# Kernel optimization log

Measured on AMD Instinct MI355X. Metric: run time of the kernel, lower is better.

Reference implementation:

```python
import jax, jax.numpy as jnp
import numpy as np
from jax import lax

B, T, D, H, HODE = 1024, 128, 64, 256, 256
DT = 0.1  # times spaced by 0.1 == integration_step_size -> one RK4 step per interval


def setup_inputs() -> dict:
    key = jax.random.key(0)
    ks = jax.random.split(key, 10)
    s = lambda fan: 1.0 / np.sqrt(fan)
    return {
        "x": jax.random.normal(ks[0], (B, T, D), jnp.float32),
        "times": jnp.arange(T, dtype=jnp.float32) * DT,
        "mask": (jax.random.uniform(ks[1], (B, T)) > 0.3).astype(jnp.float32),
        # ODE MLP: Linear(H->HODE), ReLU, Linear(HODE->H)
        "W1": jax.random.uniform(ks[2], (HODE, H), jnp.float32, -s(H), s(H)),
        "b1": jax.random.uniform(ks[3], (HODE,), jnp.float32, -s(H), s(H)),
        "W2": jax.random.uniform(ks[4], (H, HODE), jnp.float32, -s(HODE), s(HODE)),
        "b2": jax.random.uniform(ks[5], (H,), jnp.float32, -s(HODE), s(HODE)),
        # GRUCell params (torch layout: [3H, D]/[3H, H], gate order r,z,n)
        "W_ih": jax.random.uniform(ks[6], (3 * H, D), jnp.float32, -s(H), s(H)),
        "b_ih": jax.random.uniform(ks[7], (3 * H,), jnp.float32, -s(H), s(H)),
        "W_hh": jax.random.uniform(ks[8], (3 * H, H), jnp.float32, -s(H), s(H)),
        "b_hh": jax.random.uniform(ks[9], (3 * H,), jnp.float32, -s(H), s(H)),
    }


def _ode_gru_forward(x, times, mask, W1, b1, W2, b2, W_ih, b_ih, W_hh, b_hh):
    Bs, Ts, _ = x.shape
    Hs = W_hh.shape[1]

    def f(h):  # autonomous ODE vector field: MLP(h)
        return jnp.maximum(h @ W1.T + b1, 0.0) @ W2.T + b2

    def rk4_step(h, dt):
        k1 = f(h)
        k2 = f(h + 0.5 * dt * k1)
        k3 = f(h + 0.5 * dt * k2)
        k4 = f(h + dt * k3)
        return h + (dt / 6.0) * (k1 + 2.0 * k2 + 2.0 * k3 + k4)

    def gru_update(xt, h, m):
        gi = xt @ W_ih.T + b_ih  # [B, 3H]
        gh = h @ W_hh.T + b_hh
        i_r, i_z, i_n = jnp.split(gi, 3, axis=-1)
        h_r, h_z, h_n = jnp.split(gh, 3, axis=-1)
        r = jax.nn.sigmoid(i_r + h_r)
        z = jax.nn.sigmoid(i_z + h_z)
        n = jnp.tanh(i_n + r * h_n)
        h_next = (1.0 - z) * n + z * h
        m = m[:, None]
        return m * h_next + (1.0 - m) * h

    h0 = gru_update(x[:, 0], jnp.zeros((Bs, Hs), x.dtype), mask[:, 0])
    dts = times[1:] - times[:-1]  # [T-1]

    def step(h, inp):
        xt, mt, dt = inp
        h_ode = rk4_step(h, dt)
        h = gru_update(xt, h_ode, mt)
        return h, h

    xs = (jnp.swapaxes(x[:, 1:], 0, 1), jnp.swapaxes(mask[:, 1:], 0, 1), dts)
    _, hs = lax.scan(step, h0, xs)  # hs: [T-1, B, H]
    out = jnp.concatenate([h0[None], hs], axis=0)  # [T, B, H]
    return jnp.swapaxes(out, 0, 1)  # [B, T, H]


def reference(x, times, mask, W1, b1, W2, b2, W_ih, b_ih, W_hh, b_hh):
    return _ode_gru_forward(x, times, mask, W1, b1, W2, b2, W_ih, b_ih, W_hh, b_hh)
```

## Files before the change

kernel.cpp:

```cpp
#include <hip/hip_runtime.h>
#include <math.h>

#define TT_ 128
#define DD 64
#define HH 256
#define BB 16
#define NBLK 64
#define NTHR 1024

#define SA 260
#define SB 264
#define SXB 72

typedef short bf16x8 __attribute__((ext_vector_type(8)));
typedef float f32x4 __attribute__((ext_vector_type(4)));
typedef unsigned int uint;
typedef unsigned short ushort;

__device__ ushort g_W1p[16 * 8 * 2 * 512];
__device__ ushort g_W2p[16 * 8 * 2 * 512];
__device__ ushort g_Wrzp[32 * 10 * 2 * 512];
__device__ ushort g_Whnp[16 * 8 * 2 * 512];
__device__ ushort g_Winp[16 * 2 * 512];

__device__ __forceinline__ ushort bf16_rne(float f) {
  uint u = __builtin_bit_cast(uint, f);
  return (ushort)((u + 0x7fffu + ((u >> 16) & 1u)) >> 16);
}
__device__ __forceinline__ float bf16_f32(ushort h) {
  uint u = ((uint)h) << 16;
  return __builtin_bit_cast(float, u);
}
__device__ __forceinline__ void hl_split(float f, ushort& hi, ushort& lo) {
  const uint u = __builtin_bit_cast(uint, f);
  hi = (ushort)(u >> 16);
  const float fh = __builtin_bit_cast(float, u & 0xffff0000u);
  lo = (ushort)(__builtin_bit_cast(uint, f - fh) >> 16);
}

__global__ __launch_bounds__(256) void prep(
    const float* __restrict__ W1, const float* __restrict__ W2,
    const float* __restrict__ Wih, const float* __restrict__ Whh)
{
  const int s = blockIdx.x * 256 + threadIdx.x;
  const int S1 = 16 * 8 * 512;
  const int S2 = S1 + 16 * 8 * 512;
  const int S3 = S2 + 32 * 10 * 512;
  const int S4 = S3 + 16 * 8 * 512;
  const int S5 = S4 + 16 * 2 * 512;
  if (s >= S5) return;

  if (s < S2) {
    const int r = (s < S1) ? s : s - S1;
    const int t = r / (8 * 512);
    const int o = (r / 512) & 7;
    const int pos = r & 511;
    const int l = pos >> 3, j = pos & 7;
    const int n = t * 16 + (l & 15);
    const int k = o * 32 + (l >> 4) * 8 + j;
    const float w = (s < S1) ? W1[n * HH + k] : W2[n * HH + k];
    ushort hi = bf16_rne(w);
    ushort lo = bf16_rne(w - bf16_f32(hi));
    ushort* dst = (s < S1) ? g_W1p : g_W2p;
    dst[((t * 8 + o) * 2) * 512 + pos] = hi;
    dst[((t * 8 + o) * 2 + 1) * 512 + pos] = lo;
  } else if (s < S3) {
    const int r = s - S2;
    const int t = r / (10 * 512);
    const int o = (r / 512) % 10;
    const int pos = r & 511;
    const int l = pos >> 3, j = pos & 7;
    const int n = t * 16 + (l & 15);
    float w;
    if (o < 8) w = Whh[n * HH + o * 32 + (l >> 4) * 8 + j];
    else       w = Wih[n * DD + (o - 8) * 32 + (l >> 4) * 8 + j];
    ushort hi = bf16_rne(w);
    ushort lo = bf16_rne(w - bf16_f32(hi));
    g_Wrzp[((t * 10 + o) * 2) * 512 + pos] = hi;
    g_Wrzp[((t * 10 + o) * 2 + 1) * 512 + pos] = lo;
  } else if (s < S4) {
    const int r = s - S3;
    const int t = r / (8 * 512);
    const int o = (r / 512) & 7;
    const int pos = r & 511;
    const int l = pos >> 3, j = pos & 7;
    const int n = 512 + t * 16 + (l & 15);
    const float w = Whh[n * HH + o * 32 + (l >> 4) * 8 + j];
    ushort hi = bf16_rne(w);
    ushort lo = bf16_rne(w - bf16_f32(hi));
    g_Whnp[((t * 8 + o) * 2) * 512 + pos] = hi;
    g_Whnp[((t * 8 + o) * 2 + 1) * 512 + pos] = lo;
  } else {
    const int r = s - S4;
    const int t = r / (2 * 512);
    const int o = (r / 512) & 1;
    const int pos = r & 511;
    const int l = pos >> 3, j = pos & 7;
    const int n = 512 + t * 16 + (l & 15);
    const float w = Wih[n * DD + o * 32 + (l >> 4) * 8 + j];
    g_Winp[(t * 2 + o) * 512 + pos] = bf16_rne(w);
  }
}

#define MFMA(A, B, C) __builtin_amdgcn_mfma_f32_16x16x32_bf16((A), (B), (C), 0, 0, 0)

#define LBAR() asm volatile("s_waitcnt lgkmcnt(0)\ns_barrier" ::: "memory")

__device__ __forceinline__ f32x4 mm1(const ushort* __restrict__ Ahi,
                                     const ushort* __restrict__ Alo,
                                     const ushort* __restrict__ pack,
                                     int tile, int lane, f32x4 acc)
{
  const int aoff = (lane & 15) * SB + (lane >> 4) * 8;
  const ushort* wp = pack + (size_t)tile * 8192 + lane * 8;
#pragma unroll
  for (int o = 0; o < 8; ++o) {
    const bf16x8 ah = *(const bf16x8*)(Ahi + aoff + o * 32);
    const bf16x8 al = *(const bf16x8*)(Alo + aoff + o * 32);
    const bf16x8 wh = *(const bf16x8*)(wp + o * 1024);
    const bf16x8 wl = *(const bf16x8*)(wp + o * 1024 + 512);
    acc = MFMA(ah, wh, acc);
    acc = MFMA(al, wh, acc);
    acc = MFMA(ah, wl, acc);
  }
  return acc;
}

__device__ __forceinline__ void mm_rz(const ushort* __restrict__ Ahi,
                                      const ushort* __restrict__ Alo,
                                      const ushort* __restrict__ Xhi,
                                      const ushort* __restrict__ Xlo,
                                      int wv, int lane, f32x4& ar, f32x4& az)
{
  const int aoff = (lane & 15) * SB + (lane >> 4) * 8;
  const int xoff = (lane & 15) * SXB + (lane >> 4) * 8;
  const ushort* pr = g_Wrzp + (size_t)wv * 10240 + lane * 8;
  const ushort* pz = g_Wrzp + (size_t)(16 + wv) * 10240 + lane * 8;
#pragma unroll
  for (int o = 0; o < 8; ++o) {
    const bf16x8 ah = *(const bf16x8*)(Ahi + aoff + o * 32);
    const bf16x8 al = *(const bf16x8*)(Alo + aoff + o * 32);
    const bf16x8 wrh = *(const bf16x8*)(pr + o * 1024);
    const bf16x8 wrl = *(const bf16x8*)(pr + o * 1024 + 512);
    const bf16x8 wzh = *(const bf16x8*)(pz + o * 1024);
    const bf16x8 wzl = *(const bf16x8*)(pz + o * 1024 + 512);
    ar = MFMA(ah, wrh, ar); az = MFMA(ah, wzh, az);
    ar = MFMA(al, wrh, ar); az = MFMA(al, wzh, az);
    ar = MFMA(ah, wrl, ar); az = MFMA(ah, wzl, az);
  }
#pragma unroll
  for (int o = 0; o < 2; ++o) {
    const bf16x8 xh = *(const bf16x8*)(Xhi + xoff + o * 32);
    const bf16x8 xl = *(const bf16x8*)(Xlo + xoff + o * 32);
    const bf16x8 wrh = *(const bf16x8*)(pr + (8 + o) * 1024);
    const bf16x8 wzh = *(const bf16x8*)(pz + (8 + o) * 1024);
    ar = MFMA(xh, wrh, ar); az = MFMA(xh, wzh, az);
    ar = MFMA(xl, wrh, ar); az = MFMA(xl, wzh, az);
  }
}

__device__ __forceinline__ f32x4 mm_in(const ushort* __restrict__ Xhi,
                                       const ushort* __restrict__ Xlo,
                                       int wv, int lane, f32x4 acc)
{
  const int xoff = (lane & 15) * SXB + (lane >> 4) * 8;
  const ushort* pw = g_Winp + (size_t)wv * 1024 + lane * 8;
#pragma unroll
  for (int o = 0; o < 2; ++o) {
    const bf16x8 xh = *(const bf16x8*)(Xhi + xoff + o * 32);
    const bf16x8 xl = *(const bf16x8*)(Xlo + xoff + o * 32);
    const bf16x8 w = *(const bf16x8*)(pw + o * 512);
    acc = MFMA(xh, w, acc);
    acc = MFMA(xl, w, acc);
  }
  return acc;
}

__global__ __launch_bounds__(NTHR) void odegru_kernel(
    const float* __restrict__ x, const float* __restrict__ times,
    const float* __restrict__ mask,
    const float* __restrict__ b1, const float* __restrict__ b2,
    const float* __restrict__ bih, const float* __restrict__ bhh,
    float* __restrict__ out)
{
  __shared__ __align__(16) float sAh[BB * SA];
  __shared__ __align__(16) float sAin[BB * SA];
  __shared__ __align__(16) ushort sAhh[BB * SB], sAhl[BB * SB];
  __shared__ __align__(16) ushort sAinh[BB * SB], sAinl[BB * SB];
  __shared__ __align__(16) ushort sUh[BB * SB], sUl[BB * SB];
  __shared__ __align__(16) ushort sXh[BB * SXB], sXl[BB * SXB];
  __shared__ __align__(16) float sM[BB * TT_];

  const int tid = threadIdx.x;
  const int lane = tid & 63;
  const int wv = tid >> 6;
  const int l15 = lane & 15;
  const int lq = lane >> 4;
  const int b0 = blockIdx.x * BB;

  const int c = wv * 16 + l15;
  const float b1c = b1[c];
  const float b2c = b2[c];
  const float brz_r = bih[c] + bhh[c];
  const float brz_z = bih[c + 256] + bhh[c + 256];
  const float bn_i = bih[c + 512];
  const float bn_h = bhh[c + 512];

  const f32x4 Z = {0.f, 0.f, 0.f, 0.f};

  sM[tid] = mask[(size_t)b0 * TT_ + tid];
  sM[tid + 1024] = mask[(size_t)b0 * TT_ + tid + 1024];

  auto feval = [&](const ushort* Ahi, const ushort* Alo, f32x4& kv) {
    f32x4 a = mm1(Ahi, Alo, g_W1p, wv, lane, Z);
#pragma unroll
    for (int q = 0; q < 4; ++q) {
      const int b = lq * 4 + q;
      const float u = fmaxf(a[q] + b1c, 0.f);
      ushort hi, lo; hl_split(u, hi, lo);
      sUh[b * SB + c] = hi;
      sUl[b * SB + c] = lo;
    }
    LBAR();
    f32x4 p = mm1(sUh, sUl, g_W2p, wv, lane, Z);
    kv = p + b2c;
  };

  auto wAin = [&](float coef, const f32x4& v) {
#pragma unroll
    for (int q = 0; q < 4; ++q) {
      const int b = lq * 4 + q;
      const float nv = sAh[b * SA + c] + coef * v[q];
      sAin[b * SA + c] = nv;
      ushort hi, lo; hl_split(nv, hi, lo);
      sAinh[b * SB + c] = hi;
      sAinl[b * SB + c] = lo;
    }
  };

  for (int t = 0; t < TT_; ++t) {
    {
      const int b = tid >> 6, d = tid & 63;
      const float v = x[((size_t)(b0 + b) * TT_ + t) * DD + d];
      ushort hi, lo; hl_split(v, hi, lo);
      sXh[b * SXB + d] = hi;
      sXl[b * SXB + d] = lo;
    }
    if (t == 0) {
      const int cc = tid & 255;
#pragma unroll
      for (int q = 0; q < 4; ++q) {
        const int b = (tid >> 8) * 4 + q;
        sAin[b * SA + cc] = 0.f;
        sAinh[b * SB + cc] = 0;
        sAinl[b * SB + cc] = 0;
      }
    }
    LBAR();

    if (t > 0) {
      const float dtv = times[t] - times[t - 1];
      f32x4 kv, ks;
      feval(sAhh, sAhl, kv);
      ks = kv;
      wAin(0.5f * dtv, kv);
      LBAR();
      feval(sAinh, sAinl, kv);
      ks += 2.0f * kv;
      wAin(0.5f * dtv, kv);
      LBAR();
      feval(sAinh, sAinl, kv);
      ks += 2.0f * kv;
      wAin(dtv, kv);
      LBAR();
      feval(sAinh, sAinl, kv);
      ks += kv;
      wAin(dtv * (1.0f / 6.0f), ks);
      LBAR();
    }

    {
      f32x4 ar = Z, az = Z;
      mm_rz(sAinh, sAinl, sXh, sXl, wv, lane, ar, az);
      f32x4 ahn = mm1(sAinh, sAinl, g_Whnp, wv, lane, Z);
      f32x4 ain = mm_in(sXh, sXl, wv, lane, Z);

#pragma unroll
      for (int q = 0; q < 4; ++q) {
        const int b = lq * 4 + q;
        const float gr = ar[q] + brz_r;
        const float gz = az[q] + brz_z;
        const float hn = ahn[q] + bn_h;
        const float gn = ain[q] + bn_i;
        const float hode = sAin[b * SA + c];
        const float rg = 1.f / (1.f + __expf(-gr));
        const float zg = 1.f / (1.f + __expf(-gz));
        const float ng = 1.f - 2.f / (__expf(2.f * (gn + rg * hn)) + 1.f);
        const float hnext = (1.f - zg) * ng + zg * hode;
        const float m = sM[b * TT_ + t];
        const float hnew = m * hnext + (1.f - m) * hode;
        out[((size_t)(b0 + b) * TT_ + t) * HH + c] = hnew;
        sAh[b * SA + c] = hnew;
        ushort hi, lo; hl_split(hnew, hi, lo);
        sAhh[b * SB + c] = hi;
        sAhl[b * SB + c] = lo;
      }
    }
    LBAR();
  }
}

extern "C" void kernel_launch(void* const* d_in, const int* in_sizes, int n_in,
                              void* d_out, int out_size, void* d_ws, size_t ws_size,
                              hipStream_t stream) {
  (void)in_sizes; (void)n_in; (void)d_ws; (void)ws_size; (void)out_size;
  const float* x     = (const float*)d_in[0];
  const float* times = (const float*)d_in[1];
  const float* mask  = (const float*)d_in[2];
  const float* W1    = (const float*)d_in[3];
  const float* b1    = (const float*)d_in[4];
  const float* W2    = (const float*)d_in[5];
  const float* b2    = (const float*)d_in[6];
  const float* Wih   = (const float*)d_in[7];
  const float* bih   = (const float*)d_in[8];
  const float* Whh   = (const float*)d_in[9];
  const float* bhh   = (const float*)d_in[10];
  float* out = (float*)d_out;

  hipLaunchKernelGGL(prep, dim3((376832 + 255) / 256), dim3(256), 0, stream,
                     W1, W2, Wih, Whh);
  hipLaunchKernelGGL(odegru_kernel, dim3(NBLK), dim3(NTHR), 0, stream,
                     x, times, mask, b1, b2, bih, bhh, out);
}
```

Baseline: 6.858 ms.

## Prefetch packed weights each step, split MFMA accumulators, fuse GRU gate matmuls

At the start of every timestep, each wave issues global_load_lds prefetches of all its packed weight tiles into a dummy LDS buffer, so the weights are pulled into cache before the dependent MFMA chains read them from global memory. The matmul helpers now use two independent accumulators to shorten MFMA dependency chains. The r/z/n hidden-gate matmuls are fused into one loop with six accumulators, and the mask is stored transposed in LDS. The prefetches add memory traffic and instructions per step, and the extra accumulators raise register pressure.

```diff
diff --git a/kernel.cpp b/kernel.cpp
--- a/kernel.cpp
+++ b/kernel.cpp
@@ -106,74 +106,40 @@
 
 #define LBAR() asm volatile("s_waitcnt lgkmcnt(0)\ns_barrier" ::: "memory")
 
+__device__ __forceinline__ void pfq(const ushort* g, ushort* lds) {
+  __builtin_amdgcn_global_load_lds(
+      (const __attribute__((address_space(1))) void*)g,
+      (__attribute__((address_space(3))) void*)lds,
+      16, 0, 0);
+}
+__device__ __forceinline__ void pf_t16(const ushort* base, ushort* d) {
+#pragma unroll
+  for (int o = 0; o < 8; ++o) {
+    pfq(base + o * 1024, d);
+    pfq(base + o * 1024 + 512, d);
+  }
+}
+
 __device__ __forceinline__ f32x4 mm1(const ushort* __restrict__ Ahi,
                                      const ushort* __restrict__ Alo,
                                      const ushort* __restrict__ pack,
-                                     int tile, int lane, f32x4 acc)
+                                     int tile, int lane, int aoff, f32x4 acc)
 {
-  const int aoff = (lane & 15) * SB + (lane >> 4) * 8;
   const ushort* wp = pack + (size_t)tile * 8192 + lane * 8;
+  f32x4 a0 = acc;
+  f32x4 a1 = {0.f, 0.f, 0.f, 0.f};
 #pragma unroll
   for (int o = 0; o < 8; ++o) {
+    const bf16x8 wh = *(const bf16x8*)(wp + o * 1024);
+    const bf16x8 wl = *(const bf16x8*)(wp + o * 1024 + 512);
     const bf16x8 ah = *(const bf16x8*)(Ahi + aoff + o * 32);
     const bf16x8 al = *(const bf16x8*)(Alo + aoff + o * 32);
-    const bf16x8 wh = *(const bf16x8*)(wp + o * 1024);
-    const bf16x8 wl = *(const bf16x8*)(wp + o * 1024 + 512);
-    acc = MFMA(ah, wh, acc);
-    acc = MFMA(al, wh, acc);
-    acc = MFMA(ah, wl, acc);
-  }
-  return acc;
-}
-
-__device__ __forceinline__ void mm_rz(const ushort* __restrict__ Ahi,
-                                      const ushort* __restrict__ Alo,
-                                      const ushort* __restrict__ Xhi,
-                                      const ushort* __restrict__ Xlo,
-                                      int wv, int lane, f32x4& ar, f32x4& az)
-{
-  const int aoff = (lane & 15) * SB + (lane >> 4) * 8;
-  const int xoff = (lane & 15) * SXB + (lane >> 4) * 8;
-  const ushort* pr = g_Wrzp + (size_t)wv * 10240 + lane * 8;
-  const ushort* pz = g_Wrzp + (size_t)(16 + wv) * 10240 + lane * 8;
-#pragma unroll
-  for (int o = 0; o < 8; ++o) {
-    const bf16x8 ah = *(const bf16x8*)(Ahi + aoff + o * 32);
-    const bf16x8 al = *(const bf16x8*)(Alo + aoff + o * 32);
-    const bf16x8 wrh = *(const bf16x8*)(pr + o * 1024);
-    const bf16x8 wrl = *(const bf16x8*)(pr + o * 1024 + 512);
-    const bf16x8 wzh = *(const bf16x8*)(pz + o * 1024);
-    const bf16x8 wzl = *(const bf16x8*)(pz + o * 1024 + 512);
-    ar = MFMA(ah, wrh, ar); az = MFMA(ah, wzh, az);
-    ar = MFMA(al, wrh, ar); az = MFMA(al, wzh, az);
-    ar = MFMA(ah, wrl, ar); az = MFMA(ah, wzl, az);
-  }
-#pragma unroll
-  for (int o = 0; o < 2; ++o) {
-    const bf16x8 xh = *(const bf16x8*)(Xhi + xoff + o * 32);
-    const bf16x8 xl = *(const bf16x8*)(Xlo + xoff + o * 32);
-    const bf16x8 wrh = *(const bf16x8*)(pr + (8 + o) * 1024);
-    const bf16x8 wzh = *(const bf16x8*)(pz + (8 + o) * 1024);
-    ar = MFMA(xh, wrh, ar); az = MFMA(xh, wzh, az);
-    ar = MFMA(xl, wrh, ar); az = MFMA(xl, wzh, az);
-  }
-}
-
-__device__ __forceinline__ f32x4 mm_in(const ushort* __restrict__ Xhi,
-                                       const ushort* __restrict__ Xlo,
-                                       int wv, int lane, f32x4 acc)
-{
-  const int xoff = (lane & 15) * SXB + (lane >> 4) * 8;
-  const ushort* pw = g_Winp + (size_t)wv * 1024 + lane * 8;
-#pragma unroll
-  for (int o = 0; o < 2; ++o) {
-    const bf16x8 xh = *(const bf16x8*)(Xhi + xoff + o * 32);
-    const bf16x8 xl = *(const bf16x8*)(Xlo + xoff + o * 32);
-    const bf16x8 w = *(const bf16x8*)(pw + o * 512);
-    acc = MFMA(xh, w, acc);
-    acc = MFMA(xl, w, acc);
-  }
-  return acc;
+    f32x4& ac = (o & 1) ? a1 : a0;
+    ac = MFMA(ah, wh, ac);
+    ac = MFMA(al, wh, ac);
+    ac = MFMA(ah, wl, ac);
+  }
+  return a0 + a1;
 }
 
 __global__ __launch_bounds__(NTHR) void odegru_kernel(
@@ -189,7 +155,8 @@
   __shared__ __align__(16) ushort sAinh[BB * SB], sAinl[BB * SB];
   __shared__ __align__(16) ushort sUh[BB * SB], sUl[BB * SB];
   __shared__ __align__(16) ushort sXh[BB * SXB], sXl[BB * SXB];
-  __shared__ __align__(16) float sM[BB * TT_];
+  __shared__ __align__(16) float sMt[TT_ * BB];
+  __shared__ __align__(16) ushort sDummy[512];
 
   const int tid = threadIdx.x;
   const int lane = tid & 63;
@@ -197,6 +164,8 @@
   const int l15 = lane & 15;
   const int lq = lane >> 4;
   const int b0 = blockIdx.x * BB;
+  const int aoff = l15 * SB + lq * 8;
+  const int xoff = l15 * SXB + lq * 8;
 
   const int c = wv * 16 + l15;
   const float b1c = b1[c];
@@ -208,11 +177,21 @@
 
   const f32x4 Z = {0.f, 0.f, 0.f, 0.f};
 
-  sM[tid] = mask[(size_t)b0 * TT_ + tid];
-  sM[tid + 1024] = mask[(size_t)b0 * TT_ + tid + 1024];
+  const ushort* W1b = g_W1p + (size_t)wv * 8192 + lane * 8;
+  const ushort* W2b = g_W2p + (size_t)wv * 8192 + lane * 8;
+  const ushort* Wrb = g_Wrzp + (size_t)wv * 10240 + lane * 8;
+  const ushort* Wzb = g_Wrzp + (size_t)(16 + wv) * 10240 + lane * 8;
+  const ushort* Whb = g_Whnp + (size_t)wv * 8192 + lane * 8;
+  const ushort* Wib = g_Winp + (size_t)wv * 1024 + lane * 8;
+
+  {
+    const int e0 = tid, e1 = tid + 1024;
+    sMt[(e0 & 127) * BB + (e0 >> 7)] = mask[(size_t)(b0 + (e0 >> 7)) * TT_ + (e0 & 127)];
+    sMt[(e1 & 127) * BB + (e1 >> 7)] = mask[(size_t)(b0 + (e1 >> 7)) * TT_ + (e1 & 127)];
+  }
 
   auto feval = [&](const ushort* Ahi, const ushort* Alo, f32x4& kv) {
-    f32x4 a = mm1(Ahi, Alo, g_W1p, wv, lane, Z);
+    f32x4 a = mm1(Ahi, Alo, g_W1p, wv, lane, aoff, Z);
 #pragma unroll
     for (int q = 0; q < 4; ++q) {
       const int b = lq * 4 + q;
@@ -222,7 +201,7 @@
       sUl[b * SB + c] = lo;
     }
     LBAR();
-    f32x4 p = mm1(sUh, sUl, g_W2p, wv, lane, Z);
+    f32x4 p = mm1(sUh, sUl, g_W2p, wv, lane, aoff, Z);
     kv = p + b2c;
   };
 
@@ -246,6 +225,13 @@
       sXh[b * SXB + d] = hi;
       sXl[b * SXB + d] = lo;
     }
+    pf_t16(W1b, sDummy);
+    pf_t16(W2b, sDummy);
+    pf_t16(Wrb, sDummy); pfq(Wrb + 8 * 1024, sDummy); pfq(Wrb + 9 * 1024, sDummy);
+    pf_t16(Wzb, sDummy); pfq(Wzb + 8 * 1024, sDummy); pfq(Wzb + 9 * 1024, sDummy);
+    pf_t16(Whb, sDummy);
+    pfq(Wib, sDummy); pfq(Wib + 512, sDummy);
+
     if (t == 0) {
       const int cc = tid & 255;
 #pragma unroll
@@ -280,10 +266,36 @@
     }
 
     {
-      f32x4 ar = Z, az = Z;
-      mm_rz(sAinh, sAinl, sXh, sXl, wv, lane, ar, az);
-      f32x4 ahn = mm1(sAinh, sAinl, g_Whnp, wv, lane, Z);
-      f32x4 ain = mm_in(sXh, sXl, wv, lane, Z);
+      f32x4 r0 = Z, r1 = Z, z0 = Z, z1 = Z, h0 = Z, h1 = Z;
+#pragma unroll
+      for (int o = 0; o < 8; ++o) {
+        const int ac = aoff + o * 32;
+        const bf16x8 ah = *(const bf16x8*)(sAinh + ac);
+        const bf16x8 al = *(const bf16x8*)(sAinl + ac);
+        const bf16x8 wrh = *(const bf16x8*)(Wrb + o * 1024);
+        const bf16x8 wrl = *(const bf16x8*)(Wrb + o * 1024 + 512);
+        const bf16x8 wzh = *(const bf16x8*)(Wzb + o * 1024);
+        const bf16x8 wzl = *(const bf16x8*)(Wzb + o * 1024 + 512);
+        const bf16x8 whh = *(const bf16x8*)(Whb + o * 1024);
+        const bf16x8 whl = *(const bf16x8*)(Whb + o * 1024 + 512);
+        r0 = MFMA(ah, wrh, r0); r1 = MFMA(al, wrh, r1); r0 = MFMA(ah, wrl, r0);
+        z0 = MFMA(ah, wzh, z0); z1 = MFMA(al, wzh, z1); z0 = MFMA(ah, wzl, z0);
+        h0 = MFMA(ah, whh, h0); h1 = MFMA(al, whh, h1); h0 = MFMA(ah, whl, h0);
+      }
+      f32x4 ar = r0 + r1, az = z0 + z1, ahn = h0 + h1;
+      f32x4 ain = Z;
+#pragma unroll
+      for (int o = 0; o < 2; ++o) {
+        const int xc = xoff + o * 32;
+        const bf16x8 xh = *(const bf16x8*)(sXh + xc);
+        const bf16x8 xl = *(const bf16x8*)(sXl + xc);
+        const bf16x8 wr = *(const bf16x8*)(Wrb + (8 + o) * 1024);
+        const bf16x8 wz = *(const bf16x8*)(Wzb + (8 + o) * 1024);
+        const bf16x8 wi = *(const bf16x8*)(Wib + o * 512);
+        ar = MFMA(xh, wr, ar); ar = MFMA(xl, wr, ar);
+        az = MFMA(xh, wz, az); az = MFMA(xl, wz, az);
+        ain = MFMA(xh, wi, ain); ain = MFMA(xl, wi, ain);
+      }
 
 #pragma unroll
       for (int q = 0; q < 4; ++q) {
@@ -297,7 +309,7 @@
         const float zg = 1.f / (1.f + __expf(-gz));
         const float ng = 1.f - 2.f / (__expf(2.f * (gn + rg * hn)) + 1.f);
         const float hnext = (1.f - zg) * ng + zg * hode;
-        const float m = sM[b * TT_ + t];
+        const float m = sMt[t * BB + b];
         const float hnew = m * hnext + (1.f - m) * hode;
         out[((size_t)(b0 + b) * TT_ + t) * HH + c] = hnew;
         sAh[b * SA + c] = hnew;
```

After: 9.552 ms. 1.39x slower.
